# Kernel optimization log

Measured on AMD Instinct MI355X. Metric: run time of the kernel, lower is better.

Reference implementation:

```python
import jax, jax.numpy as jnp
import numpy as np
import math

B, S, D, H = 8, 4096, 1024, 16
DH = D // H  # 64

def setup_inputs() -> dict:
    key = jax.random.key(0)
    ks = jax.random.split(key, 5)
    scale = 1.0 / math.sqrt(D)
    return {
        "x": jax.random.normal(ks[0], (B, S, D), dtype=jnp.float32),
        "Wq": jax.random.normal(ks[1], (D, D), dtype=jnp.float32) * scale,
        "Wk": jax.random.normal(ks[2], (D, D), dtype=jnp.float32) * scale,
        "Wv": jax.random.normal(ks[3], (D, D), dtype=jnp.float32) * scale,
        "Wo": jax.random.normal(ks[4], (D, D), dtype=jnp.float32) * scale,
    }

def reference(x, Wq, Wk, Wv, Wo):
    # Linear layers: y = x @ W.T (torch nn.Linear convention, bias=False)
    q = x @ Wq.T  # [B,S,D]
    k = x @ Wk.T
    v = x @ Wv.T
    # split heads -> [B,H,S,DH]
    def split(t):
        return t.reshape(B, S, H, DH).transpose(0, 2, 1, 3)
    q, k, v = split(q), split(k), split(v)
    # QUIRK: scores over head-feature dims: q^T @ k -> [B,H,DH,DH]
    scores = jnp.einsum('bhsd,bhse->bhde', q, k) / math.sqrt(DH)
    att = jax.nn.softmax(scores, axis=-1)  # [B,H,DH,DH]
    # v @ att -> [B,H,S,DH]
    out = jnp.einsum('bhsd,bhde->bhse', v, att)
    out = out.transpose(0, 2, 1, 3).reshape(B, S, D)
    return out @ Wo.T  # [B,S,D]; squeeze(dim=1) is a no-op since S>1
```

## Files before the change

### kernel.cpp

```cpp
#include <hip/hip_runtime.h>
#include <hip/hip_bf16.h>


#define B_ 8
#define S_ 4096
#define D_ 1024
#define H_ 16

typedef unsigned short u16;
typedef __attribute__((ext_vector_type(4))) short short4v;
typedef __attribute__((ext_vector_type(8))) _Float16 half8v;
typedef __attribute__((ext_vector_type(4))) float f32x4;

typedef __attribute__((address_space(3))) unsigned lds_u32_t;
typedef const __attribute__((address_space(1))) unsigned glb_u32_t;

__device__ __forceinline__ unsigned short f2h(float f) {
    _Float16 h = (_Float16)f;
    return __builtin_bit_cast(unsigned short, h);
}
__device__ __forceinline__ void gll16(const u16* g, u16* lds) {
    __builtin_amdgcn_global_load_lds((glb_u32_t*)g, (lds_u32_t*)lds, 16, 0, 0);
}
__device__ __forceinline__ void pair_decode(int pair, int& ti, int& tj) {
    ti = (int)((sqrtf(8.f * pair + 1.f) - 1.f) * 0.5f);
    if ((ti + 1) * (ti + 2) / 2 <= pair) ++ti;
    if (ti * (ti + 1) / 2 > pair) --ti;
    tj = pair - ti * (ti + 1) / 2;
}

__global__ __launch_bounds__(256) void gram_splitk(
    const u16* __restrict__ xt, float* __restrict__ P)
{
    __shared__ u16 As[128 * 32];
    __shared__ u16 Bs[128 * 32];

    const int l = ((blockIdx.x & 7) * 144) + (blockIdx.x >> 3);
    const int batch = l / 144;
    const int rem = l - batch * 144;
    const int chunk = rem / 36;
    const int pair = rem - chunk * 36;
    int ti, tj;
    pair_decode(pair, ti, tj);

    const int t = threadIdx.x, lane = t & 63, wave = t >> 6;
    const int wm = (wave >> 1) * 64, wn = (wave & 1) * 64;
    const int fr = lane & 15, kg = lane >> 4;

    const u16* Ag = xt + ((long)batch * D_ + ti * 128) * S_ + chunk * 1024;
    const u16* Bg = xt + ((long)batch * D_ + tj * 128) * S_ + chunk * 1024;

    f32x4 acc[4][4];
#pragma unroll
    for (int i = 0; i < 4; ++i)
#pragma unroll
        for (int j = 0; j < 4; ++j) acc[i][j] = (f32x4){0.f, 0.f, 0.f, 0.f};

    for (int k0 = 0; k0 < 1024; k0 += 32) {
        if (k0) __syncthreads();
#pragma unroll
        for (int r = 0; r < 2; ++r) {
            const int off = r * 2048 + t * 8;
            const int row = off >> 5, kc = off & 31;
            gll16(Ag + (long)row * S_ + k0 + kc, As + off);
            gll16(Bg + (long)row * S_ + k0 + kc, Bs + off);
        }
        __syncthreads();

        const int ao = (wm + fr) * 32 + kg * 8;
        const int bo = (wn + fr) * 32 + kg * 8;
        half8v a[4], b[4];
#pragma unroll
        for (int mt = 0; mt < 4; ++mt) a[mt] = *(const half8v*)&As[ao + mt * 512];
#pragma unroll
        for (int nt = 0; nt < 4; ++nt) b[nt] = *(const half8v*)&Bs[bo + nt * 512];
#pragma unroll
        for (int mt = 0; mt < 4; ++mt)
#pragma unroll
            for (int nt = 0; nt < 4; ++nt)
                acc[mt][nt] = __builtin_amdgcn_mfma_f32_16x16x32_f16(a[mt], b[nt], acc[mt][nt], 0, 0, 0);
    }

    float* out = P + (((long)chunk * B_ + batch) * 36 + pair) * 16384;
#pragma unroll
    for (int mt = 0; mt < 4; ++mt)
#pragma unroll
        for (int nt = 0; nt < 4; ++nt)
#pragma unroll
            for (int q = 0; q < 4; ++q)
                out[(wm + mt * 16 + kg * 4 + q) * 128 + wn + nt * 16 + fr] = acc[mt][nt][q];
}

__global__ __launch_bounds__(256) void reduce_mirror(
    const float* __restrict__ P, u16* __restrict__ G)
{
    __shared__ u16 th[128][132];
    const int pair = blockIdx.x, b = blockIdx.y;
    int ti, tj;
    pair_decode(pair, ti, tj);
    const int t = threadIdx.x;
    const long tile = 16384;
    const long cs = (long)B_ * 36 * tile;
    const float* base = P + ((long)b * 36 + pair) * tile;
    u16* GB = G + (long)b * D_ * D_;

#pragma unroll
    for (int e = 0; e < 16; ++e) {
        const int idx = e * 1024 + t * 4;
        float4 s0 = *(const float4*)&base[idx];
        float4 s1 = *(const float4*)&base[cs + idx];
        float4 s2 = *(const float4*)&base[2 * cs + idx];
        float4 s3 = *(const float4*)&base[3 * cs + idx];
        float f[4] = {s0.x + s1.x + s2.x + s3.x, s0.y + s1.y + s2.y + s3.y,
                      s0.z + s1.z + s2.z + s3.z, s0.w + s1.w + s2.w + s3.w};
        const int r = idx >> 7, c = idx & 127;
        short4v hv;
#pragma unroll
        for (int j = 0; j < 4; ++j) hv[j] = (short)f2h(f[j]);
        *(short4v*)&GB[(long)(ti * 128 + r) * D_ + tj * 128 + c] = hv;
        if (ti != tj) {
#pragma unroll
            for (int j = 0; j < 4; ++j) th[c + j][r] = (u16)hv[j];
        }
    }
    if (ti != tj) {
        __syncthreads();
#pragma unroll
        for (int e = 0; e < 16; ++e) {
            const int idx = e * 1024 + t * 4;
            const int r = idx >> 7, c = idx & 127;
            short4v hv = *(const short4v*)&th[r][c];
            *(short4v*)&GB[(long)(tj * 128 + r) * D_ + ti * 128 + c] = hv;
        }
    }
}

template<int OUT>
__global__ __launch_bounds__(512) void gemm256x128(
    const u16* __restrict__ A, const u16* __restrict__ B,
    float* __restrict__ Cf, u16* __restrict__ Ch,
    int K, int lda, int ldb, int ldc, long sA, long sB, long sC)
{
    constexpr int BSZ = 12288;
    constexpr int AOF = 0, BOF = 8192;
    __shared__ u16 lds[3 * BSZ];

    const int p = blockIdx.x;
    const int l = (p & 7) * 32 + (p >> 3);
    const int bz = l >> 5;
    const int bm0 = ((l >> 3) & 3) * 256;
    const int bn0 = (l & 7) * 128;

    const int t = threadIdx.x, lane = t & 63, wave = t >> 6;
    const int wm = (wave >> 1) * 64, wn = (wave & 1) * 64;
    const int fr = lane & 15, kg = lane >> 4;
    const int xs = (fr >> 1) & 3;

    const u16* gA = A + (long)bz * sA + (long)bm0 * lda;
    const u16* gB = B + (long)bz * sB + (long)bn0 * ldb;

    f32x4 acc[4][4];
#pragma unroll
    for (int i = 0; i < 4; ++i)
#pragma unroll
        for (int j = 0; j < 4; ++j) acc[i][j] = (f32x4){0.f, 0.f, 0.f, 0.f};

    const int NT = K >> 5;

    auto stage = [&](int tt, int bs) {
        u16* base = &lds[bs * BSZ];
#pragma unroll
        for (int r = 0; r < 2; ++r) {
            const int idx = t + r * 512;
            const int row = idx >> 2, kq = idx & 3;
            const int ks = (kq ^ ((row >> 1) & 3)) << 3;
            gll16(gA + (long)row * lda + tt * 32 + ks, base + AOF + idx * 8);
        }
        {
            const int row = t >> 2, kq = t & 3;
            const int ks = (kq ^ ((row >> 1) & 3)) << 3;
            gll16(gB + (long)row * ldb + tt * 32 + ks, base + BOF + t * 8);
        }
    };

    stage(0, 0);
    stage(1, 1);
    asm volatile("s_waitcnt vmcnt(3)" ::: "memory");
    __builtin_amdgcn_s_barrier();

    for (int tt = 0; tt < NT; ++tt) {
        const u16* base = &lds[(tt % 3) * BSZ];
        if (tt + 2 < NT) stage(tt + 2, (tt + 2) % 3);

        const int ko = (kg ^ xs) << 3;
        half8v a[4], b[4];
#pragma unroll
        for (int mt = 0; mt < 4; ++mt) a[mt] = *(const half8v*)&base[AOF + (wm + mt * 16 + fr) * 32 + ko];
#pragma unroll
        for (int nt = 0; nt < 4; ++nt) b[nt] = *(const half8v*)&base[BOF + (wn + nt * 16 + fr) * 32 + ko];
#pragma unroll
        for (int mt = 0; mt < 4; ++mt)
#pragma unroll
            for (int nt = 0; nt < 4; ++nt)
                acc[mt][nt] = __builtin_amdgcn_mfma_f32_16x16x32_f16(a[mt], b[nt], acc[mt][nt], 0, 0, 0);

        if (tt + 1 < NT) {
            if (tt + 2 < NT) asm volatile("s_waitcnt vmcnt(3)" ::: "memory");
            else             asm volatile("s_waitcnt vmcnt(0)" ::: "memory");
            __builtin_amdgcn_s_barrier();
        }
    }

#pragma unroll
    for (int mt = 0; mt < 4; ++mt)
#pragma unroll
        for (int nt = 0; nt < 4; ++nt)
#pragma unroll
            for (int q = 0; q < 4; ++q) {
                const int row = bm0 + wm + mt * 16 + kg * 4 + q;
                const int col = bn0 + wn + nt * 16 + fr;
                const float v = acc[mt][nt][q];
                const long idx = (long)bz * sC + (long)row * ldc + col;
                if (OUT == 0) Cf[idx] = v;
                else Ch[idx] = f2h(v);
            }
}

__global__ __launch_bounds__(256) void scores_softmax_mfma(
    const u16* __restrict__ M, const u16* __restrict__ Wkh, float* __restrict__ att)
{
    constexpr int BSZ = 4096;
    constexpr int AOF = 0, BOF = 2048;
    __shared__ u16 lds[3 * BSZ];
    __shared__ float Sm[64][68];
    __shared__ float rowm[64], rowsv[64];

    const int bh = blockIdx.x;
    const int b = bh >> 4, h = bh & 15;
    const u16* gA = M + (long)b * D_ * D_ + (long)h * 64 * D_;
    const u16* gB = Wkh + (long)h * 64 * D_;

    const int t = threadIdx.x, lane = t & 63, wave = t >> 6;
    const int fr = lane & 15, kg = lane >> 4;
    const int xs = (fr >> 1) & 3;
    const int wrow = wave * 16;

    f32x4 acc[4];
#pragma unroll
    for (int i = 0; i < 4; ++i) acc[i] = (f32x4){0.f, 0.f, 0.f, 0.f};

    auto stage = [&](int tt, int bs) {
        u16* base = &lds[bs * BSZ];
        const int row = t >> 2, kq = t & 3;
        const int ks = (kq ^ ((row >> 1) & 3)) << 3;
        gll16(gA + (long)row * D_ + tt * 32 + ks, base + AOF + t * 8);
        gll16(gB + (long)row * D_ + tt * 32 + ks, base + BOF + t * 8);
    };

    stage(0, 0);
    stage(1, 1);
    asm volatile("s_waitcnt vmcnt(2)" ::: "memory");
    __builtin_amdgcn_s_barrier();

    const int NT = 32;
    for (int tt = 0; tt < NT; ++tt) {
        const u16* base = &lds[(tt % 3) * BSZ];
        if (tt + 2 < NT) stage(tt + 2, (tt + 2) % 3);

        const int ko = (kg ^ xs) << 3;
        half8v a = *(const half8v*)&base[AOF + (wrow + fr) * 32 + ko];
#pragma unroll
        for (int nt = 0; nt < 4; ++nt) {
            half8v bv = *(const half8v*)&base[BOF + (nt * 16 + fr) * 32 + ko];
            acc[nt] = __builtin_amdgcn_mfma_f32_16x16x32_f16(a, bv, acc[nt], 0, 0, 0);
        }

        if (tt + 1 < NT) {
            if (tt + 2 < NT) asm volatile("s_waitcnt vmcnt(2)" ::: "memory");
            else             asm volatile("s_waitcnt vmcnt(0)" ::: "memory");
            __builtin_amdgcn_s_barrier();
        }
    }

#pragma unroll
    for (int nt = 0; nt < 4; ++nt)
#pragma unroll
        for (int q = 0; q < 4; ++q)
            Sm[wrow + kg * 4 + q][nt * 16 + fr] = acc[nt][q] * 0.125f;
    __syncthreads();

    if (t < 64) {
        float m = -1e30f;
        for (int ee = 0; ee < 64; ++ee) m = fmaxf(m, Sm[t][ee]);
        float s = 0.f;
        for (int ee = 0; ee < 64; ++ee) s += expf(Sm[t][ee] - m);
        rowm[t] = m;
        rowsv[t] = 1.0f / s;
    }
    __syncthreads();
    float* abase = att + (long)bh * 4096;
#pragma unroll
    for (int dd = 0; dd < 16; ++dd) {
        const int d = (t >> 6) * 16 + dd;
        const int e = t & 63;
        abase[d * 64 + e] = expf(Sm[d][e] - rowm[d]) * rowsv[d];
    }
}

__global__ __launch_bounds__(512) void gemm256_f16(
    const u16* __restrict__ A, const u16* __restrict__ B, float* __restrict__ C,
    int K, int lda, int ldb, int ldc, long sA, long sB, long sC)
{
    __shared__ u16 lds[3][2][256 * 32];

    const int p = blockIdx.x;
    const int l = (p & 7) * 64 + (p >> 3);
    const int bz = l >> 6;
    const int bm0 = ((l >> 2) & 15) * 256;
    const int bn0 = (l & 3) * 256;

    const int t = threadIdx.x, lane = t & 63, wave = t >> 6;
    const int wm = (wave >> 2) * 128, wn = (wave & 3) * 64;
    const int fr = lane & 15, kg = lane >> 4;
    const int xr = (fr >> 1) & 3;

    const u16* Ag = A + (long)bz * sA + (long)bm0 * lda;
    const u16* Bg = B + (long)bz * sB + (long)bn0 * ldb;

    f32x4 acc[8][4];
#pragma unroll
    for (int i = 0; i < 8; ++i)
#pragma unroll
        for (int j = 0; j < 4; ++j) acc[i][j] = (f32x4){0.f, 0.f, 0.f, 0.f};

    const int NT = K >> 5;

    auto stage = [&](int tt, int bsel) {
#pragma unroll
        for (int r = 0; r < 2; ++r) {
            const int idx = t + r * 512;
            const int row = idx >> 2;
            const int kq = idx & 3;
            const int ks = (kq ^ ((row >> 1) & 3)) << 3;
            gll16(Ag + (long)row * lda + tt * 32 + ks, &lds[bsel][0][idx * 8]);
            gll16(Bg + (long)row * ldb + tt * 32 + ks, &lds[bsel][1][idx * 8]);
        }
    };

    stage(0, 0);
    stage(1, 1);
    asm volatile("s_waitcnt vmcnt(4)" ::: "memory");
    __builtin_amdgcn_s_barrier();

    for (int tt = 0; tt < NT; ++tt) {
        const int cur = tt % 3;
        if (tt + 2 < NT) stage(tt + 2, (tt + 2) % 3);

        const u16* As = &lds[cur][0][0];
        const u16* Bs = &lds[cur][1][0];
        const int ko = ((kg ^ xr) << 3);
        half8v bf[4];
#pragma unroll
        for (int nt = 0; nt < 4; ++nt)
            bf[nt] = *(const half8v*)&Bs[(wn + nt * 16 + fr) * 32 + ko];
#pragma unroll
        for (int mt = 0; mt < 8; ++mt) {
            half8v af = *(const half8v*)&As[(wm + mt * 16 + fr) * 32 + ko];
#pragma unroll
            for (int nt = 0; nt < 4; ++nt)
                acc[mt][nt] = __builtin_amdgcn_mfma_f32_16x16x32_f16(af, bf[nt], acc[mt][nt], 0, 0, 0);
        }

        if (tt + 1 < NT) {
            if (tt + 2 < NT) asm volatile("s_waitcnt vmcnt(4)" ::: "memory");
            else             asm volatile("s_waitcnt vmcnt(0)" ::: "memory");
            __builtin_amdgcn_s_barrier();
        }
    }

#pragma unroll
    for (int mt = 0; mt < 8; ++mt)
#pragma unroll
        for (int nt = 0; nt < 4; ++nt)
#pragma unroll
            for (int q = 0; q < 4; ++q) {
                const int row = bm0 + wm + mt * 16 + kg * 4 + q;
                const int col = bn0 + wn + nt * 16 + fr;
                C[(long)bz * sC + (long)row * ldc + col] = acc[mt][nt][q];
            }
}

__global__ __launch_bounds__(256) void prepack_xt(
    const float* __restrict__ x, u16* __restrict__ xt, u16* __restrict__ xh)
{
    __shared__ float tile[64][65];
    const int d0 = blockIdx.x * 64, s0 = blockIdx.y * 64, b = blockIdx.z;
    const float* xb = x + (long)b * S_ * D_;
    const int t = threadIdx.x;
    const int sr = t >> 4, dc = (t & 15) * 4;
#pragma unroll
    for (int r = 0; r < 4; ++r) {
        const int s = sr + r * 16;
        float4 v = *(const float4*)&xb[(long)(s0 + s) * D_ + d0 + dc];
        tile[dc + 0][s] = v.x;
        tile[dc + 1][s] = v.y;
        tile[dc + 2][s] = v.z;
        tile[dc + 3][s] = v.w;
        short4v hv = {(short)f2h(v.x), (short)f2h(v.y), (short)f2h(v.z), (short)f2h(v.w)};
        *(short4v*)&xh[((long)b * S_ + s0 + s) * D_ + d0 + dc] = hv;
    }
    __syncthreads();
    const int dr = t >> 4, sc = (t & 15) * 4;
    u16* tb = xt + (long)b * D_ * S_;
#pragma unroll
    for (int r = 0; r < 4; ++r) {
        const int d = dr + r * 16;
        short4v hv;
#pragma unroll
        for (int j = 0; j < 4; ++j) hv[j] = (short)f2h(tile[d][sc + j]);
        *(short4v*)&tb[(long)(d0 + d) * S_ + s0 + sc] = hv;
    }
}

__global__ __launch_bounds__(256) void convert_w(
    const float* __restrict__ Wq, const float* __restrict__ Wk, const float* __restrict__ Wo,
    u16* __restrict__ Wqh, u16* __restrict__ Wkh, u16* __restrict__ Woh)
{
    const int blk = blockIdx.x;
    const float* src;
    u16* dst;
    if (blk < 1024)      { src = Wq; dst = Wqh; }
    else if (blk < 2048) { src = Wk; dst = Wkh; }
    else                 { src = Wo; dst = Woh; }
    const long i = ((long)(blk & 1023) * 256 + threadIdx.x) * 4;
    float4 v = *(const float4*)&src[i];
    short4v hv = {(short)f2h(v.x), (short)f2h(v.y), (short)f2h(v.z), (short)f2h(v.w)};
    *(short4v*)&dst[i] = hv;
}

__global__ __launch_bounds__(256) void build_T(
    const float* __restrict__ Wv, const float* __restrict__ att, u16* __restrict__ T)
{
    __shared__ float atts[64][65];
    __shared__ float Wvs[64][65];
    const int i0 = blockIdx.x * 64, h = blockIdx.y, b = blockIdx.z;
    const int t = threadIdx.x;
    {
        int row = t >> 2, c4 = (t & 3) * 16;
        const float* ab = att + (((long)b * H_ + h) * 64) * 64;
        const float* wb = Wv + (long)h * 64 * D_ + i0;
#pragma unroll
        for (int r = 0; r < 4; ++r) {
            float4 v = *(const float4*)&ab[row * 64 + c4 + r * 4];
            atts[row][c4 + r * 4 + 0] = v.x;
            atts[row][c4 + r * 4 + 1] = v.y;
            atts[row][c4 + r * 4 + 2] = v.z;
            atts[row][c4 + r * 4 + 3] = v.w;
            float4 w = *(const float4*)&wb[(long)row * D_ + c4 + r * 4];
            Wvs[row][c4 + r * 4 + 0] = w.x;
            Wvs[row][c4 + r * 4 + 1] = w.y;
            Wvs[row][c4 + r * 4 + 2] = w.z;
            Wvs[row][c4 + r * 4 + 3] = w.w;
        }
    }
    __syncthreads();
    const int e = t & 63, ig = t >> 6;
    float acc[16];
#pragma unroll
    for (int i = 0; i < 16; ++i) acc[i] = 0.f;
#pragma unroll 8
    for (int d = 0; d < 64; ++d) {
        float av = atts[d][e];
#pragma unroll
        for (int ii = 0; ii < 16; ++ii)
            acc[ii] = fmaf(Wvs[d][ig * 16 + ii], av, acc[ii]);
    }
    u16* Tb = T + (long)b * D_ * D_;
#pragma unroll
    for (int ii = 0; ii < 16; ++ii) {
        int i = i0 + ig * 16 + ii;
        Tb[(long)i * D_ + h * 64 + e] = f2h(acc[ii]);
    }
}

extern "C" void kernel_launch(void* const* d_in, const int* in_sizes, int n_in,
                              void* d_out, int out_size, void* d_ws, size_t ws_size,
                              hipStream_t stream) {
    const float* x  = (const float*)d_in[0];
    const float* Wq = (const float*)d_in[1];
    const float* Wk = (const float*)d_in[2];
    const float* Wv = (const float*)d_in[3];
    const float* Wo = (const float*)d_in[4];
    float* out = (float*)d_out;

    const long MM = (long)D_ * D_;
    const long XE = (long)B_ * S_ * D_;
    const long GE = (long)B_ * MM;
    const long PB = 4L * B_ * 36 * 16384 * 4;

    u16* xt = (u16*)d_out;

    char* w = (char*)d_ws;
    u16* xh    = (u16*)w;   w += XE * 2;
    float* P   = (float*)w;
    u16* Mh    = (u16*)w;   w += PB;
    u16* G     = (u16*)w;   w += GE * 2;
    u16* Eth   = (u16*)w;   w += GE * 2;
    float* att = (float*)w; w += (long)B_ * H_ * 64 * 64 * 4;
    u16* Wqh   = (u16*)w;   w += MM * 2;
    u16* Woh   = (u16*)w;   w += MM * 2;
    u16* Wkh   = (u16*)w;
    u16* Th = G;

    prepack_xt<<<dim3(D_ / 64, S_ / 64, B_), 256, 0, stream>>>(x, xt, xh);
    convert_w<<<3072, 256, 0, stream>>>(Wq, Wk, Wo, Wqh, Wkh, Woh);

    gram_splitk<<<36 * 4 * B_, 256, 0, stream>>>(xt, P);

    reduce_mirror<<<dim3(36, B_), 256, 0, stream>>>(P, G);

    gemm256x128<1><<<256, 512, 0, stream>>>(
        Wqh, G, nullptr, Mh, D_, D_, D_, D_, 0, MM, MM);

    scores_softmax_mfma<<<B_ * H_, 256, 0, stream>>>(Mh, Wkh, att);

    build_T<<<dim3(D_ / 64, H_, B_), 256, 0, stream>>>(Wv, att, Th);

    gemm256x128<1><<<256, 512, 0, stream>>>(
        Woh, Th, nullptr, Eth, D_, D_, D_, D_, 0, MM, MM);

    gemm256_f16<<<(S_ / 256) * (D_ / 256) * B_, 512, 0, stream>>>(
        xh, Eth, out, D_, D_, D_, D_, (long)S_ * D_, MM, (long)S_ * D_);
}
```

Before: 302.8 us.

## Switch GEMM to K=64 tiles with double buffering and MFMA priority boost

The 256x256 fp16 GEMM now stages 64-wide K tiles into two LDS buffers, replacing 32-wide K tiles in a triple buffer. The XOR swizzle is widened to 8 chunks to match. This halves the number of barriers and loop iterations and gives each load more compute to hide behind. It also raises wave priority around the MFMA block. The trade-off is a prefetch depth of one stage instead of two and a full vmcnt(0) wait every iteration, which may expose global-load latency.

```diff
diff --git a/kernel.cpp b/kernel.cpp
--- a/kernel.cpp
+++ b/kernel.cpp
@@ -311,7 +311,7 @@
     const u16* __restrict__ A, const u16* __restrict__ B, float* __restrict__ C,
     int K, int lda, int ldb, int ldc, long sA, long sB, long sC)
 {
-    __shared__ u16 lds[3][2][256 * 32];
+    __shared__ u16 lds[2][2][256 * 64];
 
     const int p = blockIdx.x;
     const int l = (p & 7) * 64 + (p >> 3);
@@ -322,7 +322,6 @@
     const int t = threadIdx.x, lane = t & 63, wave = t >> 6;
     const int wm = (wave >> 2) * 128, wn = (wave & 3) * 64;
     const int fr = lane & 15, kg = lane >> 4;
-    const int xr = (fr >> 1) & 3;
 
     const u16* Ag = A + (long)bz * sA + (long)bm0 * lda;
     const u16* Bg = B + (long)bz * sB + (long)bn0 * ldb;
@@ -333,49 +332,55 @@
 #pragma unroll
         for (int j = 0; j < 4; ++j) acc[i][j] = (f32x4){0.f, 0.f, 0.f, 0.f};
 
-    const int NT = K >> 5;
-
-    auto stage = [&](int tt, int bsel) {
-#pragma unroll
-        for (int r = 0; r < 2; ++r) {
-            const int idx = t + r * 512;
-            const int row = idx >> 2;
-            const int kq = idx & 3;
-            const int ks = (kq ^ ((row >> 1) & 3)) << 3;
-            gll16(Ag + (long)row * lda + tt * 32 + ks, &lds[bsel][0][idx * 8]);
-            gll16(Bg + (long)row * ldb + tt * 32 + ks, &lds[bsel][1][idx * 8]);
+    const int NT = K >> 6;
+
+    auto stage = [&](int tt, int s) {
+#pragma unroll
+        for (int c = 0; c < 4; ++c) {
+            const int idx = t + c * 512;
+            const int row = idx >> 3;
+            const int kq = idx & 7;
+            const int ks = (kq ^ ((row >> 1) & 7)) << 3;
+            gll16(Ag + (long)row * lda + tt * 64 + ks, &lds[s][0][idx * 8]);
+            gll16(Bg + (long)row * ldb + tt * 64 + ks, &lds[s][1][idx * 8]);
         }
     };
 
     stage(0, 0);
-    stage(1, 1);
-    asm volatile("s_waitcnt vmcnt(4)" ::: "memory");
+    asm volatile("s_waitcnt vmcnt(0)" ::: "memory");
     __builtin_amdgcn_s_barrier();
 
     for (int tt = 0; tt < NT; ++tt) {
-        const int cur = tt % 3;
-        if (tt + 2 < NT) stage(tt + 2, (tt + 2) % 3);
+        const int cur = tt & 1;
+        if (tt + 1 < NT) stage(tt + 1, cur ^ 1);
 
         const u16* As = &lds[cur][0][0];
         const u16* Bs = &lds[cur][1][0];
-        const int ko = ((kg ^ xr) << 3);
-        half8v bf[4];
-#pragma unroll
-        for (int nt = 0; nt < 4; ++nt)
-            bf[nt] = *(const half8v*)&Bs[(wn + nt * 16 + fr) * 32 + ko];
-#pragma unroll
-        for (int mt = 0; mt < 8; ++mt) {
-            half8v af = *(const half8v*)&As[(wm + mt * 16 + fr) * 32 + ko];
-#pragma unroll
-            for (int nt = 0; nt < 4; ++nt)
-                acc[mt][nt] = __builtin_amdgcn_mfma_f32_16x16x32_f16(af, bf[nt], acc[mt][nt], 0, 0, 0);
-        }
-
-        if (tt + 1 < NT) {
-            if (tt + 2 < NT) asm volatile("s_waitcnt vmcnt(4)" ::: "memory");
-            else             asm volatile("s_waitcnt vmcnt(0)" ::: "memory");
-            __builtin_amdgcn_s_barrier();
-        }
+
+        __builtin_amdgcn_s_setprio(1);
+#pragma unroll
+        for (int ks2 = 0; ks2 < 2; ++ks2) {
+            half8v bf[4];
+#pragma unroll
+            for (int nt = 0; nt < 4; ++nt) {
+                const int row = wn + nt * 16 + fr;
+                const int off = row * 64 + (((ks2 * 4 + kg) ^ ((row >> 1) & 7)) << 3);
+                bf[nt] = *(const half8v*)&Bs[off];
+            }
+#pragma unroll
+            for (int mt = 0; mt < 8; ++mt) {
+                const int row = wm + mt * 16 + fr;
+                const int off = row * 64 + (((ks2 * 4 + kg) ^ ((row >> 1) & 7)) << 3);
+                half8v af = *(const half8v*)&As[off];
+#pragma unroll
+                for (int nt = 0; nt < 4; ++nt)
+                    acc[mt][nt] = __builtin_amdgcn_mfma_f32_16x16x32_f16(af, bf[nt], acc[mt][nt], 0, 0, 0);
+            }
+        }
+        __builtin_amdgcn_s_setprio(0);
+
+        asm volatile("s_waitcnt vmcnt(0)" ::: "memory");
+        __builtin_amdgcn_s_barrier();
     }
 
 #pragma unroll
```

New measurement: 302.2 us. About the same (-0.2%).

## Restructure final GEMM into 8-phase ping-pong pipeline with half-tile staging

Applied to the files above, without the earlier changes.

Rewrites the final 256x256 output GEMM to use K=64 tiles split into four 128-row half-tiles per buffer, with double buffering instead of triple. Each K-iteration pair is broken into eight phases that interleave LDS fragment reads, staggered global-to-LDS loads and MFMA bursts, using s_setprio and barriers. The wave-to-output mapping changes to match the new half-tile layout. The aim is better overlap of memory and matrix work in the dominant GEMM. The cost is more barriers per tile and a more fragile wait-count schedule.

```diff
diff --git a/kernel.cpp b/kernel.cpp
--- a/kernel.cpp
+++ b/kernel.cpp
@@ -307,11 +307,11 @@
     }
 }
 
-__global__ __launch_bounds__(512) void gemm256_f16(
+__global__ __launch_bounds__(512) void gemm256_8ph(
     const u16* __restrict__ A, const u16* __restrict__ B, float* __restrict__ C,
     int K, int lda, int ldb, int ldc, long sA, long sB, long sC)
 {
-    __shared__ u16 lds[3][2][256 * 32];
+    __shared__ u16 lds[2][4][128 * 64];
 
     const int p = blockIdx.x;
     const int l = (p & 7) * 64 + (p >> 3);
@@ -320,9 +320,8 @@
     const int bn0 = (l & 3) * 256;
 
     const int t = threadIdx.x, lane = t & 63, wave = t >> 6;
-    const int wm = (wave >> 2) * 128, wn = (wave & 3) * 64;
+    const int wa = wave >> 2, wb = wave & 3;
     const int fr = lane & 15, kg = lane >> 4;
-    const int xr = (fr >> 1) & 3;
 
     const u16* Ag = A + (long)bz * sA + (long)bm0 * lda;
     const u16* Bg = B + (long)bz * sB + (long)bn0 * ldb;
@@ -333,59 +332,106 @@
 #pragma unroll
         for (int j = 0; j < 4; ++j) acc[i][j] = (f32x4){0.f, 0.f, 0.f, 0.f};
 
-    const int NT = K >> 5;
-
-    auto stage = [&](int tt, int bsel) {
+    const int NT = K >> 6;
+    const int NI = NT >> 1;
+
+    auto stage_half = [&](int op, int h, int tt, int buf) {
+        if (tt >= NT) return;
+        const u16* g = op ? Bg : Ag;
+        const int ld = op ? ldb : lda;
+        u16* dst = &lds[buf][op * 2 + h][0];
 #pragma unroll
         for (int r = 0; r < 2; ++r) {
             const int idx = t + r * 512;
-            const int row = idx >> 2;
-            const int kq = idx & 3;
-            const int ks = (kq ^ ((row >> 1) & 3)) << 3;
-            gll16(Ag + (long)row * lda + tt * 32 + ks, &lds[bsel][0][idx * 8]);
-            gll16(Bg + (long)row * ldb + tt * 32 + ks, &lds[bsel][1][idx * 8]);
+            const int row = idx >> 3;
+            const int kq = idx & 7;
+            const int ks = (kq ^ ((row >> 1) & 7)) << 3;
+            gll16(g + (long)(h * 128 + row) * ld + tt * 64 + ks, dst + idx * 8);
         }
     };
 
-    stage(0, 0);
-    stage(1, 1);
+#define PHASE(QA, QB, BUF, VM, S0op, S0h, S0t, S0b, NS2, S1op, S1h, S1t, S1b)              \
+    do {                                                                                    \
+        if ((VM) == 0)      asm volatile("s_waitcnt vmcnt(0)" ::: "memory");               \
+        else if ((VM) > 0)  asm volatile("s_waitcnt vmcnt(2)" ::: "memory");               \
+        half8v av[4][2], bv[2][2];                                                          \
+        _Pragma("unroll")                                                                   \
+        for (int j = 0; j < 4; ++j) {                                                       \
+            const int mt = (QA) * 2 + (j & 1) + (j >> 1) * 4;                               \
+            const int gr = (mt & 3) * 64 + wa * 32 + (mt >> 2) * 16 + fr;                   \
+            const int r_ = gr & 127;                                                        \
+            const u16* s_ = &lds[BUF][(QA)][0];                                             \
+            _Pragma("unroll")                                                               \
+            for (int k2 = 0; k2 < 2; ++k2) {                                                \
+                const int kq = k2 * 4 + kg;                                                 \
+                av[j][k2] = *(const half8v*)&s_[r_ * 64 + ((kq ^ ((r_ >> 1) & 7)) << 3)];   \
+            }                                                                               \
+        }                                                                                   \
+        _Pragma("unroll")                                                                   \
+        for (int jn = 0; jn < 2; ++jn) {                                                    \
+            const int nt = (QB) * 2 + jn;                                                   \
+            const int gr = nt * 64 + wb * 16 + fr;                                          \
+            const int r_ = gr & 127;                                                        \
+            const u16* s_ = &lds[BUF][2 + (QB)][0];                                         \
+            _Pragma("unroll")                                                               \
+            for (int k2 = 0; k2 < 2; ++k2) {                                                \
+                const int kq = k2 * 4 + kg;                                                 \
+                bv[jn][k2] = *(const half8v*)&s_[r_ * 64 + ((kq ^ ((r_ >> 1) & 7)) << 3)];  \
+            }                                                                               \
+        }                                                                                   \
+        if ((S0op) >= 0) stage_half((S0op), (S0h), (S0t), (S0b));                           \
+        if ((NS2) > 0)   stage_half((S1op), (S1h), (S1t), (S1b));                           \
+        asm volatile("s_barrier" ::: "memory");                                             \
+        __builtin_amdgcn_s_setprio(1);                                                      \
+        _Pragma("unroll")                                                                   \
+        for (int k2 = 0; k2 < 2; ++k2)                                                      \
+            _Pragma("unroll")                                                               \
+            for (int j = 0; j < 4; ++j)                                                     \
+                _Pragma("unroll")                                                           \
+                for (int jn = 0; jn < 2; ++jn) {                                            \
+                    const int mt = (QA) * 2 + (j & 1) + (j >> 1) * 4;                       \
+                    const int nt = (QB) * 2 + jn;                                           \
+                    acc[mt][nt] = __builtin_amdgcn_mfma_f32_16x16x32_f16(                   \
+                        av[j][k2], bv[jn][k2], acc[mt][nt], 0, 0, 0);                       \
+                }                                                                           \
+        __builtin_amdgcn_s_setprio(0);                                                      \
+        asm volatile("s_barrier" ::: "memory");                                             \
+    } while (0)
+
+    stage_half(0, 0, 0, 0);
+    stage_half(1, 0, 0, 0);
+    stage_half(0, 1, 0, 0);
+    stage_half(1, 1, 0, 0);
+    stage_half(0, 0, 1, 1);
+    stage_half(1, 1, 1, 1);
     asm volatile("s_waitcnt vmcnt(4)" ::: "memory");
     __builtin_amdgcn_s_barrier();
 
-    for (int tt = 0; tt < NT; ++tt) {
-        const int cur = tt % 3;
-        if (tt + 2 < NT) stage(tt + 2, (tt + 2) % 3);
-
-        const u16* As = &lds[cur][0][0];
-        const u16* Bs = &lds[cur][1][0];
-        const int ko = ((kg ^ xr) << 3);
-        half8v bf[4];
+    for (int i = 0; i < NI; ++i) {
+        const int t1 = 2 * i + 1;
+        const int tn0 = 2 * i + 2;
+        const int tn1 = 2 * i + 3;
+        const bool last = (i == NI - 1);
+
+        PHASE(0, 0, 0, -1, 0, 1, t1, 1,  1, 1, 0, t1, 1);
+        PHASE(0, 1, 0, -1, -1, 0, 0, 0,  0, 0, 0, 0, 0);
+        PHASE(1, 1, 0, -1, 0, 0, tn0, 0, 0, 0, 0, 0, 0);
+        PHASE(1, 0, 0, last ? 0 : 2, 1, 1, tn0, 0, 0, 0, 0, 0, 0);
+        PHASE(0, 0, 1, -1, 0, 1, tn0, 0, 1, 1, 0, tn0, 0);
+        PHASE(0, 1, 1, -1, -1, 0, 0, 0,  0, 0, 0, 0, 0);
+        PHASE(1, 1, 1, -1, 0, 0, tn1, 1, 0, 0, 0, 0, 0);
+        PHASE(1, 0, 1, 2,  1, 1, tn1, 1, 0, 0, 0, 0, 0);
+    }
+#undef PHASE
+
+#pragma unroll
+    for (int mt = 0; mt < 8; ++mt)
 #pragma unroll
         for (int nt = 0; nt < 4; ++nt)
-            bf[nt] = *(const half8v*)&Bs[(wn + nt * 16 + fr) * 32 + ko];
-#pragma unroll
-        for (int mt = 0; mt < 8; ++mt) {
-            half8v af = *(const half8v*)&As[(wm + mt * 16 + fr) * 32 + ko];
-#pragma unroll
-            for (int nt = 0; nt < 4; ++nt)
-                acc[mt][nt] = __builtin_amdgcn_mfma_f32_16x16x32_f16(af, bf[nt], acc[mt][nt], 0, 0, 0);
-        }
-
-        if (tt + 1 < NT) {
-            if (tt + 2 < NT) asm volatile("s_waitcnt vmcnt(4)" ::: "memory");
-            else             asm volatile("s_waitcnt vmcnt(0)" ::: "memory");
-            __builtin_amdgcn_s_barrier();
-        }
-    }
-
-#pragma unroll
-    for (int mt = 0; mt < 8; ++mt)
-#pragma unroll
-        for (int nt = 0; nt < 4; ++nt)
 #pragma unroll
             for (int q = 0; q < 4; ++q) {
-                const int row = bm0 + wm + mt * 16 + kg * 4 + q;
-                const int col = bn0 + wn + nt * 16 + fr;
+                const int row = bm0 + (mt & 3) * 64 + wa * 32 + (mt >> 2) * 16 + kg * 4 + q;
+                const int col = bn0 + nt * 64 + wb * 16 + fr;
                 C[(long)bz * sC + (long)row * ldc + col] = acc[mt][nt][q];
             }
 }
@@ -529,6 +575,6 @@
     gemm256x128<1><<<256, 512, 0, stream>>>(
         Woh, Th, nullptr, Eth, D_, D_, D_, D_, 0, MM, MM);
 
-    gemm256_f16<<<(S_ / 256) * (D_ / 256) * B_, 512, 0, stream>>>(
+    gemm256_8ph<<<(S_ / 256) * (D_ / 256) * B_, 512, 0, stream>>>(
         xh, Eth, out, D_, D_, D_, D_, (long)S_ * D_, MM, (long)S_ * D_);
 }
```

Result: no change. 307.3 us (+1.5%).
